# Optimization experiments

Hardware: AMD Instinct MI355X
Metric: run time of the kernel (lower is better)

The kernel has to match this reference:

```python
import jax, jax.numpy as jnp
import numpy as np

N_GENES = 20000
N_CELLS = 1024   # expression_dim
FM_DIM = 512     # scgpt_embed_dim
EMB = 512        # embed_dim == projection_dim
N_EDGES = 640000
EPS = 1e-5


def _layernorm(x, g, b):
    mu = jnp.mean(x, axis=-1, keepdims=True)
    var = jnp.mean((x - mu) ** 2, axis=-1, keepdims=True)
    return (x - mu) * jax.lax.rsqrt(var + EPS) * g + b


def _sage_conv(x, src, dst, Wl, bl, Wr):
    # PyG SAGEConv (mean aggr): lin_l(mean_{j in N(i)} x_j) + lin_r(x_i)
    n = x.shape[0]
    agg = jax.ops.segment_sum(x[src], dst, num_segments=n)          # [N, F]
    cnt = jax.ops.segment_sum(jnp.ones((src.shape[0],), x.dtype), dst, num_segments=n)
    mean = agg / jnp.maximum(cnt, 1.0)[:, None]
    return mean @ Wl.T + bl + x @ Wr.T


def setup_inputs() -> dict:
    key = jax.random.key(0)
    ks = jax.random.split(key, 20)
    s = 0.02
    inp = {
        'x_foundation': jax.random.normal(ks[0], (N_GENES, FM_DIM), jnp.float32),
        'x_expression': jax.random.normal(ks[1], (N_GENES, N_CELLS), jnp.float32),
        'ppi_edge_index': jax.random.randint(ks[2], (2, N_EDGES), 0, N_GENES, jnp.int32),
        # expression SAGE layer 0 (N_CELLS -> EMB)
        'Wl0': s * jax.random.normal(ks[3], (EMB, N_CELLS), jnp.float32),
        'bl0': jnp.zeros((EMB,), jnp.float32),
        'Wr0': s * jax.random.normal(ks[4], (EMB, N_CELLS), jnp.float32),
        # expression SAGE layer 1 (EMB -> EMB)
        'Wl1': s * jax.random.normal(ks[5], (EMB, EMB), jnp.float32),
        'bl1': jnp.zeros((EMB,), jnp.float32),
        'Wr1': s * jax.random.normal(ks[6], (EMB, EMB), jnp.float32),
        # foundation projection: Linear + LayerNorm
        'Wf': s * jax.random.normal(ks[7], (EMB, FM_DIM), jnp.float32),
        'bf': jnp.zeros((EMB,), jnp.float32),
        'g1': jnp.ones((EMB,), jnp.float32),
        'b1': jnp.zeros((EMB,), jnp.float32),
        # fusion layer: Linear + LayerNorm
        'Wfu': s * jax.random.normal(ks[8], (EMB, EMB), jnp.float32),
        'bfu': jnp.zeros((EMB,), jnp.float32),
        'g2': jnp.ones((EMB,), jnp.float32),
        'b2': jnp.zeros((EMB,), jnp.float32),
        # final SAGE layer (EMB -> EMB), max(1, num_layers//2) == 1 layer
        'Wl2': s * jax.random.normal(ks[9], (EMB, EMB), jnp.float32),
        'bl2': jnp.zeros((EMB,), jnp.float32),
        'Wr2': s * jax.random.normal(ks[10], (EMB, EMB), jnp.float32),
    }
    return inp


def reference(x_foundation, x_expression, ppi_edge_index,
              Wl0, bl0, Wr0, Wl1, bl1, Wr1,
              Wf, bf, g1, b1, Wfu, bfu, g2, b2,
              Wl2, bl2, Wr2):
    src, dst = ppi_edge_index[0], ppi_edge_index[1]
    # expression branch: SAGEConv -> ELU (dropout = identity in eval)
    h = jax.nn.elu(_sage_conv(x_expression, src, dst, Wl0, bl0, Wr0))
    h = jax.nn.elu(_sage_conv(h, src, dst, Wl1, bl1, Wr1))
    # foundation branch: Linear -> LayerNorm -> GELU (exact, as torch nn.GELU)
    f = jax.nn.gelu(_layernorm(x_foundation @ Wf.T + bf, g1, b1), approximate=False)
    # add fusion, then Linear -> LayerNorm -> SiLU
    fused = h + f
    fo = jax.nn.silu(_layernorm(fused @ Wfu.T + bfu, g2, b2))
    # final SAGE layer(s): SAGEConv -> ELU
    gene_emb = jax.nn.elu(_sage_conv(fo, src, dst, Wl2, bl2, Wr2))
    return gene_emb
```

## Files before the change

kernel.cpp:

```cpp
#include <hip/hip_runtime.h>
#include <hip/hip_bf16.h>
#include <math.h>

#define N_GENES 20000
#define N_CELLS 1024
#define FM_DIM  512
#define EMB     512
#define N_EDGES 640000
#define LN_EPS  1e-5f
#define SCAN_B  79
#define IDX_CAP 2560

typedef __attribute__((ext_vector_type(8))) short bf8;
typedef __attribute__((ext_vector_type(4))) float f32x4;

__device__ __forceinline__ float bflo(unsigned v) { return __uint_as_float(v << 16); }
__device__ __forceinline__ float bfhi(unsigned v) { return __uint_as_float(v & 0xffff0000u); }
__device__ __forceinline__ unsigned short f2bf(float f) {
    unsigned u = __float_as_uint(f);
    return (unsigned short)((u + 0x7fffu + ((u >> 16) & 1u)) >> 16);
}
__device__ __forceinline__ unsigned packbf(float x, float y) {
    return (unsigned)f2bf(x) | ((unsigned)f2bf(y) << 16);
}
__device__ __forceinline__ unsigned addbf2(unsigned x, unsigned y) {
    return packbf(bflo(x) + bflo(y), bfhi(x) + bfhi(y));
}
__device__ __forceinline__ uint4 pack8(float4 a, float4 b) {
    uint4 o;
    o.x = packbf(a.x, a.y);
    o.y = packbf(a.z, a.w);
    o.z = packbf(b.x, b.y);
    o.w = packbf(b.z, b.w);
    return o;
}

__device__ __forceinline__ void gload16(const unsigned short* g, unsigned short* l) {
    __builtin_amdgcn_global_load_lds(
        (const __attribute__((address_space(1))) unsigned int*)g,
        (__attribute__((address_space(3))) unsigned int*)l, 16, 0, 0);
}

__global__ __launch_bounds__(256) void k_cvtcnt(const float4* __restrict__ xe,
                                                const float4* s0, const float4* s1,
                                                const float4* s2, const float4* s3,
                                                const float4* s4, const float4* s5,
                                                const float4* s6, const float4* s7,
                                                uint4* __restrict__ Xe,
                                                uint4* __restrict__ Wb,
                                                const int* __restrict__ edst,
                                                int* __restrict__ cnt,
                                                unsigned char* __restrict__ eslot) {
    if (blockIdx.x < 2048) {
        for (int i = blockIdx.x * 256 + threadIdx.x; i < 2560000 + 327680;
             i += 2048 * 256) {
            if (i < 2560000) {
                Xe[i] = pack8(xe[2 * i], xe[2 * i + 1]);
            } else {
                int w = i - 2560000;
                const float4* src; int off;
                if (w < 65536)       { src = s0; off = w; }
                else if (w < 131072) { src = s1; off = w - 65536; }
                else if (w < 163840) { src = s2; off = w - 131072; }
                else if (w < 196608) { src = s3; off = w - 163840; }
                else if (w < 229376) { src = s4; off = w - 196608; }
                else if (w < 262144) { src = s5; off = w - 229376; }
                else if (w < 294912) { src = s6; off = w - 262144; }
                else                 { src = s7; off = w - 294912; }
                Wb[w] = pack8(src[2 * off], src[2 * off + 1]);
            }
        }
    } else {
        int e = (blockIdx.x - 2048) * 256 + threadIdx.x;
        if (e < N_EDGES) {
            int old = atomicAdd(&cnt[edst[e]], 1);
            eslot[e] = (unsigned char)old;
        }
    }
}

__global__ __launch_bounds__(256) void k_scan1(const int* __restrict__ cnt,
                                               int* __restrict__ row_ptr,
                                               int* __restrict__ bsum) {
    __shared__ int wsum[4];
    int b = blockIdx.x, t = threadIdx.x;
    int i = b * 256 + t;
    int v = (i < N_GENES) ? cnt[i] : 0;
    int lane = t & 63, wv = t >> 6;
    int x = v;
#pragma unroll
    for (int off = 1; off < 64; off <<= 1) {
        int y = __shfl_up(x, off);
        if (lane >= off) x += y;
    }
    if (lane == 63) wsum[wv] = x;
    __syncthreads();
    if (t == 0) {
        int s = 0;
        for (int w = 0; w < 4; ++w) { int tmp = wsum[w]; wsum[w] = s; s += tmp; }
    }
    __syncthreads();
    int excl = x - v + wsum[wv];
    if (i < N_GENES) row_ptr[i] = excl;
    if (t == 255) bsum[b] = excl + v;
}

__global__ void k_scan2(const int* __restrict__ bsum, int* __restrict__ boff) {
    __shared__ int wsum[2];
    int t = threadIdx.x;
    int v = (t < SCAN_B) ? bsum[t] : 0;
    int lane = t & 63, wv = t >> 6;
    int x = v;
#pragma unroll
    for (int off = 1; off < 64; off <<= 1) {
        int y = __shfl_up(x, off);
        if (lane >= off) x += y;
    }
    if (lane == 63) wsum[wv] = x;
    __syncthreads();
    int add = (wv == 1) ? wsum[0] : 0;
    int excl = x - v + add;
    if (t < SCAN_B) boff[t] = excl;
    if (t == SCAN_B) boff[SCAN_B] = excl;
}

__global__ __launch_bounds__(256) void k_scan3(int* __restrict__ row_ptr,
                                               const int* __restrict__ boff) {
    int i = blockIdx.x * 256 + threadIdx.x;
    if (i < N_GENES) row_ptr[i] += boff[i >> 8];
    if (blockIdx.x == 0 && threadIdx.x == 0) row_ptr[N_GENES] = boff[SCAN_B];
}

__global__ __launch_bounds__(256) void k_gemm_pf(const unsigned short* __restrict__ A,
                                                 const unsigned short* __restrict__ Wl,
                                                 const unsigned short* __restrict__ Wr,
                                                 unsigned short* __restrict__ C0,
                                                 unsigned short* __restrict__ C1,
                                                 int M, int K,
                                                 const int* __restrict__ e_src,
                                                 const int* __restrict__ e_dst,
                                                 const int* __restrict__ row_ptr,
                                                 const unsigned char* __restrict__ eslot,
                                                 int* __restrict__ csr) {
    __shared__ __attribute__((aligned(16))) unsigned short As[2][128][32];
    __shared__ __attribute__((aligned(16))) unsigned short Bs[2][128][32];
    if (blockIdx.y >= 160) {
        int e = ((blockIdx.y - 160) * 8 + blockIdx.x) * 256 + threadIdx.x;
        if (e < N_EDGES) {
            int d = e_dst[e];
            csr[row_ptr[d] + (int)eslot[e]] = e_src[e];
        }
        return;
    }
    int m0 = (blockIdx.x * 20 + (blockIdx.y >> 3)) * 128;
    if (m0 >= M) return;
    int sel = blockIdx.y & 7;
    const unsigned short* W = (sel < 4) ? Wl : Wr;
    unsigned short* Cp = (sel < 4) ? C0 : C1;
    int n0 = (sel & 3) * 128;
    int tid = threadIdx.x;
    int lane = tid & 63;
    int w = tid >> 6, wr = w >> 1, wc = w & 1;

    int srow = tid >> 2, sch = tid & 3;
    int rA0 = min(m0 + srow, M - 1);
    int rA1 = min(m0 + srow + 64, M - 1);
    const unsigned short* gA0 = A + (size_t)rA0 * K + sch * 8;
    const unsigned short* gA1 = A + (size_t)rA1 * K + sch * 8;
    const unsigned short* gB0 = W + (size_t)(n0 + srow) * K + sch * 8;
    const unsigned short* gB1 = W + (size_t)(n0 + srow + 64) * K + sch * 8;

    f32x4 acc[4][4];
#pragma unroll
    for (int i = 0; i < 4; ++i)
#pragma unroll
        for (int j = 0; j < 4; ++j) acc[i][j] = (f32x4){0.f, 0.f, 0.f, 0.f};

    auto stage = [&](int b, int k0) {
        unsigned short* Ab = &As[b][0][0];
        unsigned short* Bb = &Bs[b][0][0];
        gload16(gA0 + k0, Ab + tid * 8);
        gload16(gA1 + k0, Ab + 64 * 32 + tid * 8);
        gload16(gB0 + k0, Bb + tid * 8);
        gload16(gB1 + k0, Bb + 64 * 32 + tid * 8);
    };
    auto compute = [&](int b) {
        const unsigned short* Ab = &As[b][0][0];
        const unsigned short* Bb = &Bs[b][0][0];
        bf8 af[4], bff[4];
#pragma unroll
        for (int f = 0; f < 4; ++f) {
            af[f]  = *(const bf8*)(Ab + (wr * 64 + f * 16 + (lane & 15)) * 32 + (lane >> 4) * 8);
            bff[f] = *(const bf8*)(Bb + (wc * 64 + f * 16 + (lane & 15)) * 32 + (lane >> 4) * 8);
        }
#pragma unroll
        for (int i = 0; i < 4; ++i)
#pragma unroll
            for (int j = 0; j < 4; ++j)
                acc[i][j] = __builtin_amdgcn_mfma_f32_16x16x32_bf16(af[i], bff[j],
                                                                    acc[i][j], 0, 0, 0);
    };

    const int NT = K / 32;
    stage(0, 0);
    __syncthreads();
    for (int t = 0; t < NT; t += 2) {
        stage(1, (t + 1) * 32);
        compute(0);
        __syncthreads();
        if (t + 2 < NT) stage(0, (t + 2) * 32);
        compute(1);
        __syncthreads();
    }

#pragma unroll
    for (int i = 0; i < 4; ++i) {
        int rb = m0 + wr * 64 + i * 16 + (lane >> 4) * 4;
#pragma unroll
        for (int j = 0; j < 4; ++j) {
            int cc = n0 + wc * 64 + j * 16 + (lane & 15);
#pragma unroll
            for (int e = 0; e < 4; ++e) {
                int r = rb + e;
                if (r < M) Cp[(size_t)r * EMB + cc] = f2bf(acc[i][j][e]);
            }
        }
    }
}

__global__ __launch_bounds__(256) void k_gemm_fu(const unsigned short* __restrict__ A,
                                                 const unsigned short* __restrict__ A2,
                                                 const unsigned short* __restrict__ W,
                                                 unsigned short* __restrict__ Cp,
                                                 int M, int K) {
    __shared__ __attribute__((aligned(16))) unsigned short As[2][128][32];
    __shared__ __attribute__((aligned(16))) unsigned short Bs[2][128][32];
    int m0 = (blockIdx.x * 20 + (blockIdx.y >> 2)) * 128;
    if (m0 >= M) return;
    int n0 = (blockIdx.y & 3) * 128;
    int tid = threadIdx.x;
    int lane = tid & 63;
    int w = tid >> 6, wr = w >> 1, wc = w & 1;

    int srow = tid >> 2, sch = tid & 3;
    int rA0 = min(m0 + srow, M - 1);
    int rA1 = min(m0 + srow + 64, M - 1);
    const unsigned short* gA0 = A + (size_t)rA0 * K + sch * 8;
    const unsigned short* gA1 = A + (size_t)rA1 * K + sch * 8;
    const unsigned short* hA0 = A2 + (size_t)rA0 * K + sch * 8;
    const unsigned short* hA1 = A2 + (size_t)rA1 * K + sch * 8;
    const unsigned short* gB0 = W + (size_t)(n0 + srow) * K + sch * 8;
    const unsigned short* gB1 = W + (size_t)(n0 + srow + 64) * K + sch * 8;

    f32x4 acc[4][4];
#pragma unroll
    for (int i = 0; i < 4; ++i)
#pragma unroll
        for (int j = 0; j < 4; ++j) acc[i][j] = (f32x4){0.f, 0.f, 0.f, 0.f};

    auto compute = [&](int b) {
        const unsigned short* Ab = &As[b][0][0];
        const unsigned short* Bb = &Bs[b][0][0];
        bf8 af[4], bff[4];
#pragma unroll
        for (int f = 0; f < 4; ++f) {
            af[f]  = *(const bf8*)(Ab + (wr * 64 + f * 16 + (lane & 15)) * 32 + (lane >> 4) * 8);
            bff[f] = *(const bf8*)(Bb + (wc * 64 + f * 16 + (lane & 15)) * 32 + (lane >> 4) * 8);
        }
#pragma unroll
        for (int i = 0; i < 4; ++i)
#pragma unroll
            for (int j = 0; j < 4; ++j)
                acc[i][j] = __builtin_amdgcn_mfma_f32_16x16x32_bf16(af[i], bff[j],
                                                                    acc[i][j], 0, 0, 0);
    };

    for (int k0 = 0; k0 < K; k0 += 64) {
        uint4 x00 = *(const uint4*)(gA0 + k0);
        uint4 y00 = *(const uint4*)(hA0 + k0);
        uint4 x10 = *(const uint4*)(gA1 + k0);
        uint4 y10 = *(const uint4*)(hA1 + k0);
        uint4 x01 = *(const uint4*)(gA0 + k0 + 32);
        uint4 y01 = *(const uint4*)(hA0 + k0 + 32);
        uint4 x11 = *(const uint4*)(gA1 + k0 + 32);
        uint4 y11 = *(const uint4*)(hA1 + k0 + 32);
        uint4 a00, a10, a01, a11;
        a00.x = addbf2(x00.x, y00.x); a00.y = addbf2(x00.y, y00.y);
        a00.z = addbf2(x00.z, y00.z); a00.w = addbf2(x00.w, y00.w);
        a10.x = addbf2(x10.x, y10.x); a10.y = addbf2(x10.y, y10.y);
        a10.z = addbf2(x10.z, y10.z); a10.w = addbf2(x10.w, y10.w);
        a01.x = addbf2(x01.x, y01.x); a01.y = addbf2(x01.y, y01.y);
        a01.z = addbf2(x01.z, y01.z); a01.w = addbf2(x01.w, y01.w);
        a11.x = addbf2(x11.x, y11.x); a11.y = addbf2(x11.y, y11.y);
        a11.z = addbf2(x11.z, y11.z); a11.w = addbf2(x11.w, y11.w);
        __syncthreads();
        *(uint4*)(&As[0][0][0] + tid * 8)       = a00;
        *(uint4*)(&As[0][64][0] + tid * 8)      = a10;
        *(uint4*)(&As[1][0][0] + tid * 8)       = a01;
        *(uint4*)(&As[1][64][0] + tid * 8)      = a11;
        gload16(gB0 + k0,      &Bs[0][0][0] + tid * 8);
        gload16(gB1 + k0,      &Bs[0][64][0] + tid * 8);
        gload16(gB0 + k0 + 32, &Bs[1][0][0] + tid * 8);
        gload16(gB1 + k0 + 32, &Bs[1][64][0] + tid * 8);
        __syncthreads();
        compute(0);
        compute(1);
    }

#pragma unroll
    for (int i = 0; i < 4; ++i) {
        int rb = m0 + wr * 64 + i * 16 + (lane >> 4) * 4;
#pragma unroll
        for (int j = 0; j < 4; ++j) {
            int cc = n0 + wc * 64 + j * 16 + (lane & 15);
#pragma unroll
            for (int e = 0; e < 4; ++e) {
                int r = rb + e;
                if (r < M) Cp[(size_t)r * EMB + cc] = f2bf(acc[i][j][e]);
            }
        }
    }
}

__global__ __launch_bounds__(256) void k_gemm_p(const unsigned short* __restrict__ A,
                                                const unsigned short* __restrict__ Wl,
                                                const unsigned short* __restrict__ Wr,
                                                unsigned short* __restrict__ C0,
                                                unsigned short* __restrict__ C1,
                                                int M, int K) {
    __shared__ __attribute__((aligned(16))) unsigned short As[2][128][32];
    __shared__ __attribute__((aligned(16))) unsigned short Bs[2][128][32];
    int m0 = (blockIdx.x * 20 + (blockIdx.y >> 3)) * 128;
    if (m0 >= M) return;
    int sel = blockIdx.y & 7;
    const unsigned short* W = (sel < 4) ? Wl : Wr;
    unsigned short* Cp = (sel < 4) ? C0 : C1;
    int n0 = (sel & 3) * 128;
    int tid = threadIdx.x;
    int lane = tid & 63;
    int w = tid >> 6, wr = w >> 1, wc = w & 1;

    int srow = tid >> 2, sch = tid & 3;
    int rA0 = min(m0 + srow, M - 1);
    int rA1 = min(m0 + srow + 64, M - 1);
    const unsigned short* gA0 = A + (size_t)rA0 * K + sch * 8;
    const unsigned short* gA1 = A + (size_t)rA1 * K + sch * 8;
    const unsigned short* gB0 = W + (size_t)(n0 + srow) * K + sch * 8;
    const unsigned short* gB1 = W + (size_t)(n0 + srow + 64) * K + sch * 8;

    f32x4 acc[4][4];
#pragma unroll
    for (int i = 0; i < 4; ++i)
#pragma unroll
        for (int j = 0; j < 4; ++j) acc[i][j] = (f32x4){0.f, 0.f, 0.f, 0.f};

    auto compute = [&](int b) {
        const unsigned short* Ab = &As[b][0][0];
        const unsigned short* Bb = &Bs[b][0][0];
        bf8 af[4], bff[4];
#pragma unroll
        for (int f = 0; f < 4; ++f) {
            af[f]  = *(const bf8*)(Ab + (wr * 64 + f * 16 + (lane & 15)) * 32 + (lane >> 4) * 8);
            bff[f] = *(const bf8*)(Bb + (wc * 64 + f * 16 + (lane & 15)) * 32 + (lane >> 4) * 8);
        }
#pragma unroll
        for (int i = 0; i < 4; ++i)
#pragma unroll
            for (int j = 0; j < 4; ++j)
                acc[i][j] = __builtin_amdgcn_mfma_f32_16x16x32_bf16(af[i], bff[j],
                                                                    acc[i][j], 0, 0, 0);
    };

    for (int k0 = 0; k0 < K; k0 += 64) {
        __syncthreads();
        gload16(gA0 + k0,      &As[0][0][0] + tid * 8);
        gload16(gA1 + k0,      &As[0][64][0] + tid * 8);
        gload16(gA0 + k0 + 32, &As[1][0][0] + tid * 8);
        gload16(gA1 + k0 + 32, &As[1][64][0] + tid * 8);
        gload16(gB0 + k0,      &Bs[0][0][0] + tid * 8);
        gload16(gB1 + k0,      &Bs[0][64][0] + tid * 8);
        gload16(gB0 + k0 + 32, &Bs[1][0][0] + tid * 8);
        gload16(gB1 + k0 + 32, &Bs[1][64][0] + tid * 8);
        __syncthreads();
        compute(0);
        compute(1);
    }

#pragma unroll
    for (int i = 0; i < 4; ++i) {
        int rb = m0 + wr * 64 + i * 16 + (lane >> 4) * 4;
#pragma unroll
        for (int j = 0; j < 4; ++j) {
            int cc = n0 + wc * 64 + j * 16 + (lane & 15);
#pragma unroll
            for (int e = 0; e < 4; ++e) {
                int r = rb + e;
                if (r < M) Cp[(size_t)r * EMB + cc] = f2bf(acc[i][j][e]);
            }
        }
    }
}

__global__ __launch_bounds__(256) void k_gemm_3(const unsigned short* __restrict__ A1,
                                                const float* __restrict__ A2,
                                                const unsigned short* __restrict__ Wl,
                                                const unsigned short* __restrict__ Wr,
                                                const unsigned short* __restrict__ Wf,
                                                unsigned short* __restrict__ C0,
                                                unsigned short* __restrict__ C1,
                                                unsigned short* __restrict__ CF,
                                                int M) {
    const int K = 512;
    __shared__ __attribute__((aligned(16))) unsigned short As[2][128][32];
    __shared__ __attribute__((aligned(16))) unsigned short Bs[2][128][32];
    int y = blockIdx.y;
    bool fpath = (y >= 160);
    int m0, n0;
    const unsigned short* W;
    unsigned short* Cp;
    if (!fpath) {
        m0 = (blockIdx.x * 20 + (y >> 3)) * 128;
        int sel = y & 7;
        W = (sel < 4) ? Wl : Wr;
        Cp = (sel < 4) ? C0 : C1;
        n0 = (sel & 3) * 128;
    } else {
        int y2 = y - 160;
        m0 = (blockIdx.x * 20 + (y2 >> 2)) * 128;
        n0 = (y2 & 3) * 128;
        W = Wf;
        Cp = CF;
    }
    if (m0 >= M) return;
    int tid = threadIdx.x;
    int lane = tid & 63;
    int w = tid >> 6, wr = w >> 1, wc = w & 1;

    int srow = tid >> 2, sch = tid & 3;
    int rA0 = min(m0 + srow, M - 1);
    int rA1 = min(m0 + srow + 64, M - 1);
    const unsigned short* gA0 = A1 + (size_t)rA0 * K + sch * 8;
    const unsigned short* gA1 = A1 + (size_t)rA1 * K + sch * 8;
    const float* fA0 = A2 + (size_t)rA0 * K + sch * 8;
    const float* fA1 = A2 + (size_t)rA1 * K + sch * 8;
    const unsigned short* gB0 = W + (size_t)(n0 + srow) * K + sch * 8;
    const unsigned short* gB1 = W + (size_t)(n0 + srow + 64) * K + sch * 8;

    f32x4 acc[4][4];
#pragma unroll
    for (int i = 0; i < 4; ++i)
#pragma unroll
        for (int j = 0; j < 4; ++j) acc[i][j] = (f32x4){0.f, 0.f, 0.f, 0.f};

    auto compute = [&](int b) {
        const unsigned short* Ab = &As[b][0][0];
        const unsigned short* Bb = &Bs[b][0][0];
        bf8 af[4], bff[4];
#pragma unroll
        for (int f = 0; f < 4; ++f) {
            af[f]  = *(const bf8*)(Ab + (wr * 64 + f * 16 + (lane & 15)) * 32 + (lane >> 4) * 8);
            bff[f] = *(const bf8*)(Bb + (wc * 64 + f * 16 + (lane & 15)) * 32 + (lane >> 4) * 8);
        }
#pragma unroll
        for (int i = 0; i < 4; ++i)
#pragma unroll
            for (int j = 0; j < 4; ++j)
                acc[i][j] = __builtin_amdgcn_mfma_f32_16x16x32_bf16(af[i], bff[j],
                                                                    acc[i][j], 0, 0, 0);
    };

    for (int k0 = 0; k0 < K; k0 += 64) {
        float4 f0a, f0b, f0c, f0d, f1a, f1b, f1c, f1d;
        if (fpath) {
            f0a = *(const float4*)(fA0 + k0);      f0b = *(const float4*)(fA0 + k0 + 4);
            f1a = *(const float4*)(fA1 + k0);      f1b = *(const float4*)(fA1 + k0 + 4);
            f0c = *(const float4*)(fA0 + k0 + 32); f0d = *(const float4*)(fA0 + k0 + 36);
            f1c = *(const float4*)(fA1 + k0 + 32); f1d = *(const float4*)(fA1 + k0 + 36);
        }
        __syncthreads();
        if (fpath) {
            *(uint4*)(&As[0][0][0] + tid * 8)  = pack8(f0a, f0b);
            *(uint4*)(&As[0][64][0] + tid * 8) = pack8(f1a, f1b);
            *(uint4*)(&As[1][0][0] + tid * 8)  = pack8(f0c, f0d);
            *(uint4*)(&As[1][64][0] + tid * 8) = pack8(f1c, f1d);
        } else {
            gload16(gA0 + k0,      &As[0][0][0] + tid * 8);
            gload16(gA1 + k0,      &As[0][64][0] + tid * 8);
            gload16(gA0 + k0 + 32, &As[1][0][0] + tid * 8);
            gload16(gA1 + k0 + 32, &As[1][64][0] + tid * 8);
        }
        gload16(gB0 + k0,      &Bs[0][0][0] + tid * 8);
        gload16(gB1 + k0,      &Bs[0][64][0] + tid * 8);
        gload16(gB0 + k0 + 32, &Bs[1][0][0] + tid * 8);
        gload16(gB1 + k0 + 32, &Bs[1][64][0] + tid * 8);
        __syncthreads();
        compute(0);
        compute(1);
    }

#pragma unroll
    for (int i = 0; i < 4; ++i) {
        int rb = m0 + wr * 64 + i * 16 + (lane >> 4) * 4;
#pragma unroll
        for (int j = 0; j < 4; ++j) {
            int cc = n0 + wc * 64 + j * 16 + (lane & 15);
#pragma unroll
            for (int e = 0; e < 4; ++e) {
                int r = rb + e;
                if (r < M) Cp[(size_t)r * EMB + cc] = f2bf(acc[i][j][e]);
            }
        }
    }
}

template <int OUTF32>
__device__ __forceinline__ void sage_body(const unsigned short* yl,
                                          const unsigned short* yr,
                                          const float* bl,
                                          const int* row_ptr,
                                          const int* csr,
                                          void* outp, int slice, int nblk,
                                          int* sIdx) {
    int g = threadIdx.x >> 3;
    int l = threadIdx.x & 7;
    int node = nblk * 32 + g;
    int w = slice * 8 + l;
    int s32 = row_ptr[nblk * 32];
    int e32 = row_ptr[nblk * 32 + 32];
    int nIdx = e32 - s32;
    bool lds_ok = (nIdx <= IDX_CAP);
    if (lds_ok) {
        for (int i = threadIdx.x; i < nIdx; i += 256) sIdx[i] = csr[s32 + i];
    }
    __syncthreads();
    int s = row_ptr[node], e = row_ptr[node + 1];
    int deg = e - s;
    const char* Yb = (const char*)yl;
    unsigned lb = (unsigned)(w << 4);
    float ac[8];
#pragma unroll
    for (int q = 0; q < 8; ++q) ac[q] = 0.f;
    if (lds_ok) {
        int lp = s - s32;
        int p = 0;
        for (; p + 8 <= deg; p += 8) {
            int j[8];
#pragma unroll
            for (int q = 0; q < 8; ++q) j[q] = sIdx[lp + p + q];
            uint4 v[8];
#pragma unroll
            for (int q = 0; q < 8; ++q)
                v[q] = *(const uint4*)(Yb + (((unsigned)j[q] << 10) + lb));
#pragma unroll
            for (int q = 0; q < 8; ++q) {
                ac[0] += bflo(v[q].x); ac[1] += bfhi(v[q].x);
                ac[2] += bflo(v[q].y); ac[3] += bfhi(v[q].y);
                ac[4] += bflo(v[q].z); ac[5] += bfhi(v[q].z);
                ac[6] += bflo(v[q].w); ac[7] += bfhi(v[q].w);
            }
        }
        for (; p < deg; ++p) {
            int j = sIdx[lp + p];
            uint4 v = *(const uint4*)(Yb + (((unsigned)j << 10) + lb));
            ac[0] += bflo(v.x); ac[1] += bfhi(v.x);
            ac[2] += bflo(v.y); ac[3] += bfhi(v.y);
            ac[4] += bflo(v.z); ac[5] += bfhi(v.z);
            ac[6] += bflo(v.w); ac[7] += bfhi(v.w);
        }
    } else {
        for (int p = s; p < e; ++p) {
            int j = csr[p];
            uint4 v = *(const uint4*)(Yb + (((unsigned)j << 10) + lb));
            ac[0] += bflo(v.x); ac[1] += bfhi(v.x);
            ac[2] += bflo(v.y); ac[3] += bfhi(v.y);
            ac[4] += bflo(v.z); ac[5] += bfhi(v.z);
            ac[6] += bflo(v.w); ac[7] += bfhi(v.w);
        }
    }
    float inv = 1.f / fmaxf((float)deg, 1.f);
    uint4 vr = ((const uint4*)yr)[(size_t)node * 64 + w];
    float4 bA = ((const float4*)bl)[2 * w];
    float4 bB = ((const float4*)bl)[2 * w + 1];
    float o[8];
    o[0] = ac[0] * inv + bA.x + bflo(vr.x);
    o[1] = ac[1] * inv + bA.y + bfhi(vr.x);
    o[2] = ac[2] * inv + bA.z + bflo(vr.y);
    o[3] = ac[3] * inv + bA.w + bfhi(vr.y);
    o[4] = ac[4] * inv + bB.x + bflo(vr.z);
    o[5] = ac[5] * inv + bB.y + bfhi(vr.z);
    o[6] = ac[6] * inv + bB.z + bflo(vr.w);
    o[7] = ac[7] * inv + bB.w + bfhi(vr.w);
#pragma unroll
    for (int q = 0; q < 8; ++q) o[q] = o[q] > 0.f ? o[q] : expm1f(o[q]);
    if (OUTF32) {
        float4* O = (float4*)outp;
        O[(size_t)node * 128 + 2 * w]     = make_float4(o[0], o[1], o[2], o[3]);
        O[(size_t)node * 128 + 2 * w + 1] = make_float4(o[4], o[5], o[6], o[7]);
    } else {
        uint4 ov;
        ov.x = packbf(o[0], o[1]);
        ov.y = packbf(o[2], o[3]);
        ov.z = packbf(o[4], o[5]);
        ov.w = packbf(o[6], o[7]);
        ((uint4*)outp)[(size_t)node * 64 + w] = ov;
    }
}

template <int OUTF32>
__global__ __launch_bounds__(256) void k_sage_b(const unsigned short* __restrict__ yl,
                                                const unsigned short* __restrict__ yr,
                                                const float* __restrict__ bl,
                                                const int* __restrict__ row_ptr,
                                                const int* __restrict__ csr,
                                                void* __restrict__ outp) {
    __shared__ int sIdx[IDX_CAP];
    sage_body<OUTF32>(yl, yr, bl, row_ptr, csr, outp, blockIdx.x, blockIdx.y, sIdx);
}

template <int ACT>
__device__ __forceinline__ void ln_body(const unsigned short* X,
                                        const float* bias, const float* g,
                                        const float* b, unsigned short* Y, int row) {
    __shared__ float red[8];
    int t = threadIdx.x;
    unsigned v = *(const unsigned*)(X + (size_t)row * EMB + 2 * t);
    float x0 = bflo(v) + bias[2 * t];
    float x1 = bfhi(v) + bias[2 * t + 1];
    float s = x0 + x1;
    float q = x0 * x0 + x1 * x1;
#pragma unroll
    for (int off = 32; off > 0; off >>= 1) {
        s += __shfl_down(s, off);
        q += __shfl_down(q, off);
    }
    int wave = t >> 6, lane = t & 63;
    if (lane == 0) { red[wave * 2] = s; red[wave * 2 + 1] = q; }
    __syncthreads();
    if (t == 0) {
        float ts = 0.f, tq = 0.f;
        for (int w = 0; w < 4; w++) { ts += red[w * 2]; tq += red[w * 2 + 1]; }
        red[0] = ts; red[1] = tq;
    }
    __syncthreads();
    float mu   = red[0] * (1.0f / 512.0f);
    float var  = red[1] * (1.0f / 512.0f) - mu * mu;
    float rstd = rsqrtf(var + LN_EPS);
    float y0 = (x0 - mu) * rstd * g[2 * t]     + b[2 * t];
    float y1 = (x1 - mu) * rstd * g[2 * t + 1] + b[2 * t + 1];
    if (ACT == 0) {
        y0 = 0.5f * y0 * (1.0f + erff(y0 * 0.70710678118654752440f));
        y1 = 0.5f * y1 * (1.0f + erff(y1 * 0.70710678118654752440f));
    } else {
        y0 = y0 / (1.0f + expf(-y0));
        y1 = y1 / (1.0f + expf(-y1));
    }
    ((unsigned*)Y)[(size_t)row * (EMB / 2) + t] = packbf(y0, y1);
}

template <int ACT>
__global__ __launch_bounds__(256) void k_ln_b(const unsigned short* __restrict__ X,
                                              const float* __restrict__ bias,
                                              const float* __restrict__ g,
                                              const float* __restrict__ b,
                                              unsigned short* __restrict__ Y) {
    ln_body<ACT>(X, bias, g, b, Y, blockIdx.x);
}

__global__ __launch_bounds__(256) void k_sageln(const unsigned short* __restrict__ C0,
                                                const unsigned short* __restrict__ C1,
                                                const float* __restrict__ bl1,
                                                const int* __restrict__ row_ptr,
                                                const int* __restrict__ csr,
                                                unsigned short* __restrict__ Pd,
                                                const unsigned short* __restrict__ F0,
                                                const float* __restrict__ bf_,
                                                const float* __restrict__ g1,
                                                const float* __restrict__ b1,
                                                unsigned short* __restrict__ fout) {
    __shared__ int sIdx[IDX_CAP];
    if (blockIdx.y < 625) {
        sage_body<0>(C0, C1, bl1, row_ptr, csr, Pd, blockIdx.x, blockIdx.y, sIdx);
    } else {
        ln_body<0>(F0, bf_, g1, b1, fout, (blockIdx.y - 625) * 8 + blockIdx.x);
    }
}

extern "C" void kernel_launch(void* const* d_in, const int* in_sizes, int n_in,
                              void* d_out, int out_size, void* d_ws, size_t ws_size,
                              hipStream_t stream) {
    const float* x_found = (const float*)d_in[0];
    const float* x_exp   = (const float*)d_in[1];
    const int*   ppi     = (const int*)d_in[2];
    const float* Wl0 = (const float*)d_in[3];
    const float* bl0 = (const float*)d_in[4];
    const float* Wr0 = (const float*)d_in[5];
    const float* Wl1 = (const float*)d_in[6];
    const float* bl1 = (const float*)d_in[7];
    const float* Wr1 = (const float*)d_in[8];
    const float* Wf  = (const float*)d_in[9];
    const float* bf_ = (const float*)d_in[10];
    const float* g1  = (const float*)d_in[11];
    const float* b1  = (const float*)d_in[12];
    const float* Wfu = (const float*)d_in[13];
    const float* bfu = (const float*)d_in[14];
    const float* g2  = (const float*)d_in[15];
    const float* b2  = (const float*)d_in[16];
    const float* Wl2 = (const float*)d_in[17];
    const float* bl2 = (const float*)d_in[18];
    const float* Wr2 = (const float*)d_in[19];

    const int* e_src = ppi;
    const int* e_dst = ppi + N_EDGES;

    char* ws = (char*)d_ws;
    unsigned short* C0   = (unsigned short*)(ws);
    unsigned short* C1   = (unsigned short*)(ws + 20480000);
    unsigned short* actA = (unsigned short*)(ws + 40960000);
    int* cnt     = (int*)(ws + 61440000);
    int* row_ptr = (int*)(ws + 61520000);
    unsigned char* eslot = (unsigned char*)(ws + 61600064);
    int* csr     = (int*)(ws + 62240064);
    unsigned short* Wb = (unsigned short*)(ws + 64800064);
    unsigned short* Wl0b = Wb;
    unsigned short* Wr0b = Wb + 524288;
    unsigned short* Wl1b = Wb + 1048576;
    unsigned short* Wr1b = Wb + 1310720;
    unsigned short* Wfb  = Wb + 1572864;
    unsigned short* Wfub = Wb + 1835008;
    unsigned short* Wl2b = Wb + 2097152;
    unsigned short* Wr2b = Wb + 2359296;
    int* bsum = (int*)(ws + 70042944);
    int* boff = (int*)(ws + 70043264);

    unsigned short* Xe = (unsigned short*)d_out;
    unsigned short* Pd = (unsigned short*)d_out;
    unsigned short* F0 = (unsigned short*)d_out + 10240000;

    hipMemsetAsync(cnt, 0, N_GENES * sizeof(int), stream);
    k_cvtcnt<<<4548, 256, 0, stream>>>((const float4*)x_exp,
                                       (const float4*)Wl0, (const float4*)Wr0,
                                       (const float4*)Wl1, (const float4*)Wr1,
                                       (const float4*)Wf,  (const float4*)Wfu,
                                       (const float4*)Wl2, (const float4*)Wr2,
                                       (uint4*)Xe, (uint4*)Wb, e_dst, cnt, eslot);
    k_scan1<<<SCAN_B, 256, 0, stream>>>(cnt, row_ptr, bsum);
    k_scan2<<<1, 128, 0, stream>>>(bsum, boff);
    k_scan3<<<SCAN_B, 256, 0, stream>>>(row_ptr, boff);

    dim3 gg(8, 80);
    dim3 gp(8, 160);
    dim3 g3(8, 240);
    dim3 gpf(8, 473);
    dim3 gs(8, 625);
    dim3 gsl(8, 3125);

    k_gemm_pf<<<gpf, 256, 0, stream>>>(Xe, Wl0b, Wr0b, C0, C1, N_GENES, N_CELLS,
                                       e_src, e_dst, row_ptr, eslot, csr);
    k_sage_b<0><<<gs, 256, 0, stream>>>(C0, C1, bl0, row_ptr, csr, actA);

    k_gemm_3<<<g3, 256, 0, stream>>>(actA, x_found, Wl1b, Wr1b, Wfb,
                                     C0, C1, F0, N_GENES);
    k_sageln<<<gsl, 256, 0, stream>>>(C0, C1, bl1, row_ptr, csr,
                                      Pd, F0, bf_, g1, b1, actA);

    k_gemm_fu<<<gg, 256, 0, stream>>>(Pd, actA, Wfub, C0, N_GENES, EMB);
    k_ln_b<1><<<N_GENES, 256, 0, stream>>>(C0, bfu, g2, b2, actA);

    k_gemm_p<<<gp, 256, 0, stream>>>(actA, Wl2b, Wr2b, C0, C1, N_GENES, EMB);
    k_sage_b<1><<<gs, 256, 0, stream>>>(C0, C1, bl2, row_ptr, csr, (float*)d_out);
}
```

Baseline: 414.9 us.

## Triple-buffer LDS tiles in the projection GEMM with explicit vmcnt waits

```diff
diff --git a/kernel.cpp b/kernel.cpp
--- a/kernel.cpp
+++ b/kernel.cpp
@@ -142,8 +142,8 @@
                                                  const int* __restrict__ row_ptr,
                                                  const unsigned char* __restrict__ eslot,
                                                  int* __restrict__ csr) {
-    __shared__ __attribute__((aligned(16))) unsigned short As[2][128][32];
-    __shared__ __attribute__((aligned(16))) unsigned short Bs[2][128][32];
+    __shared__ __attribute__((aligned(16))) unsigned short As[3][128][32];
+    __shared__ __attribute__((aligned(16))) unsigned short Bs[3][128][32];
     if (blockIdx.y >= 160) {
         int e = ((blockIdx.y - 160) * 8 + blockIdx.x) * 256 + threadIdx.x;
         if (e < N_EDGES) {
@@ -201,17 +201,36 @@
                                                                     acc[i][j], 0, 0, 0);
     };
 
+#define PF_STEP(CB, SB, ST, VM)                                  \
+    stage(SB, (ST) * 32);                                        \
+    asm volatile("s_waitcnt vmcnt(" #VM ")" ::: "memory");       \
+    __builtin_amdgcn_s_barrier();                                \
+    __builtin_amdgcn_sched_barrier(0);                           \
+    compute(CB);                                                 \
+    asm volatile("s_waitcnt lgkmcnt(0)" ::: "memory");           \
+    __builtin_amdgcn_s_barrier();                                \
+    __builtin_amdgcn_sched_barrier(0);
+
     const int NT = K / 32;
     stage(0, 0);
-    __syncthreads();
-    for (int t = 0; t < NT; t += 2) {
-        stage(1, (t + 1) * 32);
-        compute(0);
-        __syncthreads();
-        if (t + 2 < NT) stage(0, (t + 2) * 32);
-        compute(1);
-        __syncthreads();
-    }
+    stage(1, 32);
+    for (int t = 0; t + 4 < NT; t += 3) {
+        PF_STEP(0, 2, t + 2, 8)
+        PF_STEP(1, 0, t + 3, 8)
+        PF_STEP(2, 1, t + 4, 8)
+    }
+    asm volatile("s_waitcnt vmcnt(4)" ::: "memory");
+    __builtin_amdgcn_s_barrier();
+    __builtin_amdgcn_sched_barrier(0);
+    compute(0);
+    asm volatile("s_waitcnt lgkmcnt(0)" ::: "memory");
+    __builtin_amdgcn_s_barrier();
+    __builtin_amdgcn_sched_barrier(0);
+    asm volatile("s_waitcnt vmcnt(0)" ::: "memory");
+    __builtin_amdgcn_s_barrier();
+    __builtin_amdgcn_sched_barrier(0);
+    compute(1);
+#undef PF_STEP
 
 #pragma unroll
     for (int i = 0; i < 4; ++i) {
```

After: 413.7 us (median of 3 runs). Within noise of the previous version (-0.3%).
